# Kernel tuning notes

Hardware: AMD Instinct MI355X
Metric: run time of the kernel (lower is better)

## Reference

```python
import jax, jax.numpy as jnp
import numpy as np

BETA = 0.95
THR = 1.0
SLOPE = 25.0


@jax.custom_vjp
def spike(x):
    # heaviside(x) with fast_sigmoid surrogate gradient (slope=25)
    return (x > 0).astype(x.dtype)

def _spike_fwd(x):
    return (x > 0).astype(x.dtype), x

def _spike_bwd(x, g):
    return (g / (SLOPE * jnp.abs(x) + 1.0) ** 2,)

spike.defvjp(_spike_fwd, _spike_bwd)


def setup_inputs() -> dict:
    key = jax.random.key(0)
    ks = jax.random.split(key, 16)
    T, B, D_in, H, C = 25, 128, 2048, 4096, 1000
    P_ACTIVE = 0.1

    def sparse_layer(kw, kb, km, fan_in, fan_out):
        bound = (6.0 / fan_in) ** 0.5  # kaiming_uniform with a=sqrt(5) -> U(-sqrt(6/fan_in)*?, ...); approx scale
        w = jax.random.uniform(kw, (fan_out, fan_in), minval=-bound, maxval=bound, dtype=jnp.float32)
        mask = (jax.random.uniform(km, (fan_out, fan_in)) < P_ACTIVE).astype(jnp.float32)
        # rescale rows by sqrt(fan_in / fan_in_active) on active weights
        fan_act = jnp.clip(mask.sum(axis=1, keepdims=True), 1.0, None)
        scale = jnp.where((fan_act > 0) & (fan_act < fan_in), (fan_in / fan_act) ** 0.5, 1.0)
        w = jnp.where(mask > 0, w * scale, w)
        fan_eff = jnp.maximum(mask.sum(axis=1).mean(), 1.0)
        b_bound = 1.0 / fan_eff ** 0.5
        b = jax.random.uniform(kb, (fan_out,), minval=-b_bound, maxval=b_bound, dtype=jnp.float32)
        return w, b, mask

    w1, b1, m1 = sparse_layer(ks[0], ks[1], ks[2], D_in, H)
    w2, b2, m2 = sparse_layer(ks[3], ks[4], ks[5], H, H)
    w3, b3, m3 = sparse_layer(ks[6], ks[7], ks[8], H, H)
    bo_bound = 1.0 / H ** 0.5
    w_out = jax.random.uniform(ks[9], (C, H), minval=-bo_bound, maxval=bo_bound, dtype=jnp.float32)
    b_out = jax.random.uniform(ks[10], (C,), minval=-bo_bound, maxval=bo_bound, dtype=jnp.float32)
    x_seq = jax.random.normal(ks[11], (T, B, D_in), dtype=jnp.float32)
    return {"x_seq": x_seq, "w1": w1, "b1": b1, "m1": m1, "w2": w2, "b2": b2, "m2": m2,
            "w3": w3, "b3": b3, "m3": m3, "w_out": w_out, "b_out": b_out}


def _lif(cur, mem):
    # snntorch Leaky, reset_mechanism='subtract': reset spike from PREVIOUS mem, detached
    reset = jax.lax.stop_gradient((mem > THR).astype(mem.dtype))
    mem_new = BETA * mem + cur - reset * THR
    spk = spike(mem_new - THR)
    return spk, mem_new


def reference(x_seq, w1, b1, m1, w2, b2, m2, w3, b3, m3, w_out, b_out):
    T, B, _ = x_seq.shape
    ew1 = w1 * m1  # effective weights cached once (math identical to per-step recompute)
    ew2 = w2 * m2
    ew3 = w3 * m3

    mem1 = jnp.zeros((B, ew1.shape[0]), x_seq.dtype)
    mem2 = jnp.zeros((B, ew2.shape[0]), x_seq.dtype)
    mem3 = jnp.zeros((B, ew3.shape[0]), x_seq.dtype)
    mem_o = jnp.zeros((B, w_out.shape[0]), x_seq.dtype)
    spk_sum = jnp.zeros((B, w_out.shape[0]), x_seq.dtype)

    def step(carry, x_t):
        mem1, mem2, mem3, mem_o, spk_sum = carry
        spk1, mem1 = _lif(x_t @ ew1.T + b1, mem1)
        spk2, mem2 = _lif(spk1 @ ew2.T + b2, mem2)
        spk3, mem3 = _lif(spk2 @ ew3.T + b3, mem3)
        spk_o, mem_o = _lif(spk3 @ w_out.T + b_out, mem_o)
        return (mem1, mem2, mem3, mem_o, spk_sum + spk_o), None

    (mem1, mem2, mem3, mem_o, spk_sum), _ = jax.lax.scan(
        step, (mem1, mem2, mem3, mem_o, spk_sum), x_seq)
    return spk_sum
```

## Files before the change

kernel.cpp:

```cpp
#include <hip/hip_runtime.h>

#define T_STEPS 25
#define BATCH   128
#define D_IN    2048
#define H_DIM   4096
#define C_DIM   1000
#define N_ALL   3200
#define GEMM_Q  320
#define P_K2048 7
#define P_K4096 13
#define WOT_LD  1024

typedef __attribute__((address_space(1))) const void gas_t;
typedef __attribute__((address_space(3))) void las_t;

__device__ __forceinline__ int panel_len(int rem) {
    return (rem >= 2 * GEMM_Q) ? GEMM_Q
         : (rem > GEMM_Q ? ((rem / 2 + 15) & ~15) : rem);
}

__global__ __launch_bounds__(256)
void tmask_k(float* __restrict__ dst, const float* __restrict__ src,
             const float* __restrict__ msk, int M, int K, int MT)
{
    __shared__ float t[32][33];
    const int tx = threadIdx.x, ty = threadIdx.y;
    const int k0 = blockIdx.x * 32, m0 = blockIdx.y * 32;
    #pragma unroll
    for (int i = 0; i < 4; ++i) {
        const int m = m0 + ty + 8 * i;
        float v = 0.f;
        if (m < M) {
            const size_t gi = (size_t)m * K + k0 + tx;
            v = src[gi];
            if (msk) v *= msk[gi];
        }
        t[ty + 8 * i][tx] = v;
    }
    __syncthreads();
    const int mc = m0 + tx;
    if (mc < MT) {
        #pragma unroll
        for (int i = 0; i < 4; ++i)
            dst[(size_t)(k0 + ty + 8 * i) * MT + mc] = t[tx][ty + 8 * i];
    }
}

#define FMAQ(AS, R)                                                   \
    acc[R].x = fmaf(AS, bv.x, acc[R].x);                              \
    acc[R].y = fmaf(AS, bv.y, acc[R].y);                              \
    acc[R].z = fmaf(AS, bv.z, acc[R].z);                              \
    acc[R].w = fmaf(AS, bv.w, acc[R].w);

__global__ __launch_bounds__(256)
void gemm_w(const float* __restrict__ AT, const float* __restrict__ B,
            float* __restrict__ part, int MT, int K, int ldb, int n0)
{
#pragma clang fp reassociate(off)
    __shared__ __align__(16) float Bs[2][16][128];
    __shared__ __align__(16) float As[4][2][16][16];
    const int tid  = threadIdx.x;
    const int w    = tid >> 6;
    const int lane = tid & 63;
    const int mg   = lane >> 5;
    const int lc   = lane & 31;
    const int m0   = blockIdx.y * 64 + w * 16;
    const int p    = blockIdx.x;

    int pstart = 0, rem = K, pl = panel_len(K);
    for (int i = 0; i < p; ++i) { pstart += pl; rem -= pl; pl = panel_len(rem); }
    const int nt = pl >> 4;

    float4 acc[8];
    #pragma unroll
    for (int r = 0; r < 8; ++r) acc[r] = make_float4(0.f, 0.f, 0.f, 0.f);

    const int akr = lane >> 2, amq = (lane & 3) * 4;
    const float* ap = AT + (size_t)(pstart + akr) * MT + m0 + amq;
    const float* bsrc = B + (size_t)(pstart + w * 4 + (lane >> 5)) * ldb + n0 + lc * 4;

    {
        __builtin_amdgcn_global_load_lds((gas_t*)ap, (las_t*)&As[w][0][0][0], 16, 0, 0);
        __builtin_amdgcn_global_load_lds((gas_t*)bsrc,
                                         (las_t*)&Bs[0][w * 4][0], 16, 0, 0);
        __builtin_amdgcn_global_load_lds((gas_t*)(bsrc + 2 * (size_t)ldb),
                                         (las_t*)&Bs[0][w * 4 + 2][0], 16, 0, 0);
    }
    __syncthreads();

    for (int ti = 0; ti < nt; ++ti) {
        const int bf = ti & 1;
        if (ti + 1 < nt) {
            const float* a2 = ap + (size_t)(ti + 1) * 16 * MT;
            const float* b2 = bsrc + (size_t)(ti + 1) * 16 * ldb;
            __builtin_amdgcn_global_load_lds((gas_t*)a2, (las_t*)&As[w][bf ^ 1][0][0], 16, 0, 0);
            __builtin_amdgcn_global_load_lds((gas_t*)b2,
                                             (las_t*)&Bs[bf ^ 1][w * 4][0], 16, 0, 0);
            __builtin_amdgcn_global_load_lds((gas_t*)(b2 + 2 * (size_t)ldb),
                                             (las_t*)&Bs[bf ^ 1][w * 4 + 2][0], 16, 0, 0);
        }
        {
            float4 a0 = *(const float4*)&As[w][bf][0][mg * 8];
            float4 a1 = *(const float4*)&As[w][bf][0][mg * 8 + 4];
            float4 bv = *(const float4*)&Bs[bf][0][lc * 4];
            #pragma unroll
            for (int kk = 0; kk < 16; ++kk) {
                float4 na0, na1, nbv;
                if (kk < 15) {
                    na0 = *(const float4*)&As[w][bf][kk + 1][mg * 8];
                    na1 = *(const float4*)&As[w][bf][kk + 1][mg * 8 + 4];
                    nbv = *(const float4*)&Bs[bf][kk + 1][lc * 4];
                }
                FMAQ(a0.x, 0) FMAQ(a0.y, 1) FMAQ(a0.z, 2) FMAQ(a0.w, 3)
                FMAQ(a1.x, 4) FMAQ(a1.y, 5) FMAQ(a1.z, 6) FMAQ(a1.w, 7)
                if (kk < 15) { a0 = na0; a1 = na1; bv = nbv; }
            }
        }
        __syncthreads();
    }

    const int mrow0 = m0 + mg * 8;
    #pragma unroll
    for (int r = 0; r < 8; ++r)
        *(float4*)&part[((size_t)p * MT + mrow0 + r) * BATCH + lc * 4] = acc[r];
}

__device__ __forceinline__ float lif1e(float c, float& m)
{
    const float r = (m > 1.0f) ? 1.0f : 0.0f;
    const float mn = __fsub_rn(__fadd_rn(__fmul_rn(0.95f, m), c), r);
    m = mn;
    return (mn > 1.0f) ? 1.0f : 0.0f;
}

__global__ __launch_bounds__(256)
void reduce_lif4(const float* __restrict__ part, int P, int Mdim,
                 const float* __restrict__ bias, float* __restrict__ mem,
                 float* __restrict__ spk)
{
#pragma clang fp reassociate(off)
    const int idx4 = blockIdx.x * 256 + threadIdx.x;
    const int idx = idx4 * 4;
    const size_t stride = (size_t)Mdim * BATCH;
    float4 tot = *(const float4*)&part[idx];
    for (int z = 1; z < P; ++z) {
        const float4 pv = *(const float4*)&part[(size_t)z * stride + idx];
        tot.x = __fadd_rn(tot.x, pv.x); tot.y = __fadd_rn(tot.y, pv.y);
        tot.z = __fadd_rn(tot.z, pv.z); tot.w = __fadd_rn(tot.w, pv.w);
    }
    const float bb = bias[idx >> 7];
    float4 mm = *(float4*)&mem[idx];
    float4 sp;
    sp.x = lif1e(__fadd_rn(tot.x, bb), mm.x);
    sp.y = lif1e(__fadd_rn(tot.y, bb), mm.y);
    sp.z = lif1e(__fadd_rn(tot.z, bb), mm.z);
    sp.w = lif1e(__fadd_rn(tot.w, bb), mm.w);
    *(float4*)&mem[idx] = mm;
    *(float4*)&spk[idx] = sp;
}

__global__ __launch_bounds__(256)
void reduce_lif_out4(const float* __restrict__ part, int P, int Mpad,
                     const float* __restrict__ bias, float* __restrict__ mem,
                     float* __restrict__ out)
{
#pragma clang fp reassociate(off)
    const int idx4 = blockIdx.x * 256 + threadIdx.x;
    if (idx4 >= (C_DIM * BATCH) / 4) return;
    const int idx = idx4 * 4;
    const int cc = idx >> 7, b = idx & 127;
    const size_t stride = (size_t)Mpad * BATCH;
    float4 tot = *(const float4*)&part[idx];
    for (int z = 1; z < P; ++z) {
        const float4 pv = *(const float4*)&part[(size_t)z * stride + idx];
        tot.x = __fadd_rn(tot.x, pv.x); tot.y = __fadd_rn(tot.y, pv.y);
        tot.z = __fadd_rn(tot.z, pv.z); tot.w = __fadd_rn(tot.w, pv.w);
    }
    const float bb = bias[cc];
    float4 mm = *(float4*)&mem[idx];
    float s;
    s = lif1e(__fadd_rn(tot.x, bb), mm.x); if (s > 0.f) out[(size_t)(b+0) * C_DIM + cc] += 1.0f;
    s = lif1e(__fadd_rn(tot.y, bb), mm.y); if (s > 0.f) out[(size_t)(b+1) * C_DIM + cc] += 1.0f;
    s = lif1e(__fadd_rn(tot.z, bb), mm.z); if (s > 0.f) out[(size_t)(b+2) * C_DIM + cc] += 1.0f;
    s = lif1e(__fadd_rn(tot.w, bb), mm.w); if (s > 0.f) out[(size_t)(b+3) * C_DIM + cc] += 1.0f;
    *(float4*)&mem[idx] = mm;
}

extern "C" void kernel_launch(void* const* d_in, const int* in_sizes, int n_in,
                              void* d_out, int out_size, void* d_ws, size_t ws_size,
                              hipStream_t stream)
{
    const float* x  = (const float*)d_in[0];
    const float* w1 = (const float*)d_in[1];
    const float* b1 = (const float*)d_in[2];
    const float* m1 = (const float*)d_in[3];
    const float* w2 = (const float*)d_in[4];
    const float* b2 = (const float*)d_in[5];
    const float* m2 = (const float*)d_in[6];
    const float* w3 = (const float*)d_in[7];
    const float* b3 = (const float*)d_in[8];
    const float* m3 = (const float*)d_in[9];
    const float* wo = (const float*)d_in[10];
    const float* bo = (const float*)d_in[11];
    float* out = (float*)d_out;
    float* ws  = (float*)d_ws;
    (void)in_sizes; (void)n_in; (void)ws_size;

    const size_t HB = (size_t)H_DIM * BATCH;
    const size_t CB = (size_t)C_DIM * BATCH;

    size_t off = 0;
    const size_t MEM1 = off; off += HB;
    const size_t MEM2 = off; off += HB;
    const size_t MEM3 = off; off += HB;
    const size_t MEMO = off; off += CB;
    const size_t stateFloats = off;
    const size_t SPK1 = off; off += HB;
    const size_t SPK2 = off; off += HB;
    const size_t SPK3 = off; off += HB;
    const size_t PART = off; off += (size_t)P_K4096 * HB;
    const size_t EWT1 = off; off += (size_t)D_IN * H_DIM;
    const size_t EWT2 = off; off += (size_t)H_DIM * H_DIM;
    const size_t EWT3 = off; off += (size_t)H_DIM * H_DIM;
    const size_t WOT  = off; off += (size_t)H_DIM * WOT_LD;
    const size_t XT   = off; off += (size_t)D_IN * N_ALL;

    hipMemsetAsync(d_ws, 0, stateFloats * sizeof(float), stream);
    hipMemsetAsync(d_out, 0, (size_t)out_size * sizeof(float), stream);

    {
        dim3 tb(32, 8);
        tmask_k<<<dim3(D_IN / 32, H_DIM / 32), tb, 0, stream>>>(ws + EWT1, w1, m1, H_DIM, D_IN, H_DIM);
        tmask_k<<<dim3(H_DIM / 32, H_DIM / 32), tb, 0, stream>>>(ws + EWT2, w2, m2, H_DIM, H_DIM, H_DIM);
        tmask_k<<<dim3(H_DIM / 32, H_DIM / 32), tb, 0, stream>>>(ws + EWT3, w3, m3, H_DIM, H_DIM, H_DIM);
        tmask_k<<<dim3(H_DIM / 32, WOT_LD / 32), tb, 0, stream>>>(ws + WOT, wo, nullptr, C_DIM, H_DIM, WOT_LD);
        tmask_k<<<dim3(D_IN / 32, N_ALL / 32), tb, 0, stream>>>(ws + XT, x, nullptr, N_ALL, D_IN, N_ALL);
    }

    const dim3 g1(P_K2048, H_DIM / 64);
    const dim3 g23(P_K4096, H_DIM / 64);
    const dim3 go(P_K4096, WOT_LD / 64);
    const int gLif4  = (int)(HB / 4 / 256);
    const int gLifO4 = (int)((CB / 4 + 255) / 256);

    for (int t = 0; t < T_STEPS; ++t) {
        gemm_w<<<g1, 256, 0, stream>>>(ws + EWT1, ws + XT, ws + PART,
                                       H_DIM, D_IN, N_ALL, t * BATCH);
        reduce_lif4<<<gLif4, 256, 0, stream>>>(ws + PART, P_K2048, H_DIM, b1, ws + MEM1, ws + SPK1);

        gemm_w<<<g23, 256, 0, stream>>>(ws + EWT2, ws + SPK1, ws + PART,
                                        H_DIM, H_DIM, BATCH, 0);
        reduce_lif4<<<gLif4, 256, 0, stream>>>(ws + PART, P_K4096, H_DIM, b2, ws + MEM2, ws + SPK2);

        gemm_w<<<g23, 256, 0, stream>>>(ws + EWT3, ws + SPK2, ws + PART,
                                        H_DIM, H_DIM, BATCH, 0);
        reduce_lif4<<<gLif4, 256, 0, stream>>>(ws + PART, P_K4096, H_DIM, b3, ws + MEM3, ws + SPK3);

        gemm_w<<<go, 256, 0, stream>>>(ws + WOT, ws + SPK3, ws + PART,
                                       WOT_LD, H_DIM, BATCH, 0);
        reduce_lif_out4<<<gLifO4, 256, 0, stream>>>(ws + PART, P_K4096, WOT_LD, bo, ws + MEMO, out);
    }
}
```

Baseline: 5.164 ms.

## Co-launch next step's layer-1 GEMM with output GEMM and pair their reductions

Layer 1 depends only on the input sequence, so its GEMM for step t+1 is merged into one launch with the output-layer GEMM of step t. Their reduce/LIF kernels are likewise merged into one launch. The aim is to fill the GPU better, since the output GEMM has few blocks, and to cut per-step launch count. This needs a separate partial buffer region for the output layer so the two partial sums do not collide. It also adds a prologue GEMM before the loop and an epilogue reduction after it.

```diff
diff --git a/kernel.cpp b/kernel.cpp
--- a/kernel.cpp
+++ b/kernel.cpp
@@ -52,20 +52,23 @@
     acc[R].z = fmaf(AS, bv.z, acc[R].z);                              \
     acc[R].w = fmaf(AS, bv.w, acc[R].w);
 
-__global__ __launch_bounds__(256)
-void gemm_w(const float* __restrict__ AT, const float* __restrict__ B,
-            float* __restrict__ part, int MT, int K, int ldb, int n0)
+typedef float BsT[16][128];
+typedef float AsT[2][16][16];
+
+__device__ __forceinline__ void gemm_body(BsT* Bs, AsT* As,
+                                          const float* __restrict__ AT,
+                                          const float* __restrict__ B,
+                                          float* __restrict__ part,
+                                          int MT, int K, int ldb, int n0,
+                                          int p, int my)
 {
 #pragma clang fp reassociate(off)
-    __shared__ __align__(16) float Bs[2][16][128];
-    __shared__ __align__(16) float As[4][2][16][16];
     const int tid  = threadIdx.x;
     const int w    = tid >> 6;
     const int lane = tid & 63;
     const int mg   = lane >> 5;
     const int lc   = lane & 31;
-    const int m0   = blockIdx.y * 64 + w * 16;
-    const int p    = blockIdx.x;
+    const int m0   = my * 64 + w * 16;
 
     int pstart = 0, rem = K, pl = panel_len(K);
     for (int i = 0; i < p; ++i) { pstart += pl; rem -= pl; pl = panel_len(rem); }
@@ -125,6 +128,33 @@
         *(float4*)&part[((size_t)p * MT + mrow0 + r) * BATCH + lc * 4] = acc[r];
 }
 
+__global__ __launch_bounds__(256)
+void gemm_w(const float* __restrict__ AT, const float* __restrict__ B,
+            float* __restrict__ part, int MT, int K, int ldb, int n0)
+{
+    __shared__ __align__(16) float BsS[2][16][128];
+    __shared__ __align__(16) float AsS[4][2][16][16];
+    gemm_body((BsT*)BsS, (AsT*)AsS, AT, B, part, MT, K, ldb, n0,
+              blockIdx.x, blockIdx.y);
+}
+
+__global__ __launch_bounds__(256)
+void gemm_pair(const float* __restrict__ ATo, const float* __restrict__ Bo,
+               float* __restrict__ po, int MTo, int Ko, int ldbo, int n0o, int nbo, int npo,
+               const float* __restrict__ AT1, const float* __restrict__ B1,
+               float* __restrict__ p1, int MT1, int K1, int ldb1, int n01, int np1)
+{
+    __shared__ __align__(16) float BsS[2][16][128];
+    __shared__ __align__(16) float AsS[4][2][16][16];
+    const int bid = blockIdx.x;
+    if (bid < nbo)
+        gemm_body((BsT*)BsS, (AsT*)AsS, ATo, Bo, po, MTo, Ko, ldbo, n0o,
+                  bid % npo, bid / npo);
+    else
+        gemm_body((BsT*)BsS, (AsT*)AsS, AT1, B1, p1, MT1, K1, ldb1, n01,
+                  (bid - nbo) % np1, (bid - nbo) / np1);
+}
+
 __device__ __forceinline__ float lif1e(float c, float& m)
 {
     const float r = (m > 1.0f) ? 1.0f : 0.0f;
@@ -133,13 +163,12 @@
     return (mn > 1.0f) ? 1.0f : 0.0f;
 }
 
-__global__ __launch_bounds__(256)
-void reduce_lif4(const float* __restrict__ part, int P, int Mdim,
-                 const float* __restrict__ bias, float* __restrict__ mem,
-                 float* __restrict__ spk)
+__device__ __forceinline__ void red_lif4_body(int bid, const float* __restrict__ part,
+                                              int P, int Mdim, const float* __restrict__ bias,
+                                              float* __restrict__ mem, float* __restrict__ spk)
 {
 #pragma clang fp reassociate(off)
-    const int idx4 = blockIdx.x * 256 + threadIdx.x;
+    const int idx4 = bid * 256 + threadIdx.x;
     const int idx = idx4 * 4;
     const size_t stride = (size_t)Mdim * BATCH;
     float4 tot = *(const float4*)&part[idx];
@@ -159,13 +188,12 @@
     *(float4*)&spk[idx] = sp;
 }
 
-__global__ __launch_bounds__(256)
-void reduce_lif_out4(const float* __restrict__ part, int P, int Mpad,
-                     const float* __restrict__ bias, float* __restrict__ mem,
-                     float* __restrict__ out)
+__device__ __forceinline__ void red_lifo_body(int bid, const float* __restrict__ part,
+                                              int P, int Mpad, const float* __restrict__ bias,
+                                              float* __restrict__ mem, float* __restrict__ out)
 {
 #pragma clang fp reassociate(off)
-    const int idx4 = blockIdx.x * 256 + threadIdx.x;
+    const int idx4 = bid * 256 + threadIdx.x;
     if (idx4 >= (C_DIM * BATCH) / 4) return;
     const int idx = idx4 * 4;
     const int cc = idx >> 7, b = idx & 127;
@@ -184,6 +212,32 @@
     s = lif1e(__fadd_rn(tot.z, bb), mm.z); if (s > 0.f) out[(size_t)(b+2) * C_DIM + cc] += 1.0f;
     s = lif1e(__fadd_rn(tot.w, bb), mm.w); if (s > 0.f) out[(size_t)(b+3) * C_DIM + cc] += 1.0f;
     *(float4*)&mem[idx] = mm;
+}
+
+__global__ __launch_bounds__(256)
+void reduce_lif4(const float* __restrict__ part, int P, int Mdim,
+                 const float* __restrict__ bias, float* __restrict__ mem,
+                 float* __restrict__ spk)
+{ red_lif4_body(blockIdx.x, part, P, Mdim, bias, mem, spk); }
+
+__global__ __launch_bounds__(256)
+void reduce_lif_out4(const float* __restrict__ part, int P, int Mpad,
+                     const float* __restrict__ bias, float* __restrict__ mem,
+                     float* __restrict__ out)
+{ red_lifo_body(blockIdx.x, part, P, Mpad, bias, mem, out); }
+
+__global__ __launch_bounds__(256)
+void reduce_pair(const float* __restrict__ part, int P, int Mdim,
+                 const float* __restrict__ bias, float* __restrict__ mem,
+                 float* __restrict__ spk,
+                 const float* __restrict__ parto, int Po, int Mpad,
+                 const float* __restrict__ biaso, float* __restrict__ memo,
+                 float* __restrict__ outp, int nb1)
+{
+    if ((int)blockIdx.x < nb1)
+        red_lif4_body(blockIdx.x, part, P, Mdim, bias, mem, spk);
+    else
+        red_lifo_body(blockIdx.x - nb1, parto, Po, Mpad, biaso, memo, outp);
 }
 
 extern "C" void kernel_launch(void* const* d_in, const int* in_sizes, int n_in,
@@ -219,6 +273,7 @@
     const size_t SPK2 = off; off += HB;
     const size_t SPK3 = off; off += HB;
     const size_t PART = off; off += (size_t)P_K4096 * HB;
+    const size_t PARTO = PART + (size_t)P_K2048 * HB;
     const size_t EWT1 = off; off += (size_t)D_IN * H_DIM;
     const size_t EWT2 = off; off += (size_t)H_DIM * H_DIM;
     const size_t EWT3 = off; off += (size_t)H_DIM * H_DIM;
@@ -242,22 +297,31 @@
     const dim3 go(P_K4096, WOT_LD / 64);
     const int gLif4  = (int)(HB / 4 / 256);
     const int gLifO4 = (int)((CB / 4 + 255) / 256);
+    const int NB_OUT = P_K4096 * (WOT_LD / 64);
+    const int NB_L1  = P_K2048 * (H_DIM / 64);
+
+    gemm_w<<<g1, 256, 0, stream>>>(ws + EWT1, ws + XT, ws + PART, H_DIM, D_IN, N_ALL, 0);
 
     for (int t = 0; t < T_STEPS; ++t) {
-        gemm_w<<<g1, 256, 0, stream>>>(ws + EWT1, ws + XT, ws + PART,
-                                       H_DIM, D_IN, N_ALL, t * BATCH);
-        reduce_lif4<<<gLif4, 256, 0, stream>>>(ws + PART, P_K2048, H_DIM, b1, ws + MEM1, ws + SPK1);
-
-        gemm_w<<<g23, 256, 0, stream>>>(ws + EWT2, ws + SPK1, ws + PART,
-                                        H_DIM, H_DIM, BATCH, 0);
+        if (t == 0)
+            reduce_lif4<<<gLif4, 256, 0, stream>>>(ws + PART, P_K2048, H_DIM, b1, ws + MEM1, ws + SPK1);
+        else
+            reduce_pair<<<gLif4 + gLifO4, 256, 0, stream>>>(
+                ws + PART, P_K2048, H_DIM, b1, ws + MEM1, ws + SPK1,
+                ws + PARTO, P_K4096, WOT_LD, bo, ws + MEMO, out, gLif4);
+
+        gemm_w<<<g23, 256, 0, stream>>>(ws + EWT2, ws + SPK1, ws + PART, H_DIM, H_DIM, BATCH, 0);
         reduce_lif4<<<gLif4, 256, 0, stream>>>(ws + PART, P_K4096, H_DIM, b2, ws + MEM2, ws + SPK2);
 
-        gemm_w<<<g23, 256, 0, stream>>>(ws + EWT3, ws + SPK2, ws + PART,
-                                        H_DIM, H_DIM, BATCH, 0);
+        gemm_w<<<g23, 256, 0, stream>>>(ws + EWT3, ws + SPK2, ws + PART, H_DIM, H_DIM, BATCH, 0);
         reduce_lif4<<<gLif4, 256, 0, stream>>>(ws + PART, P_K4096, H_DIM, b3, ws + MEM3, ws + SPK3);
 
-        gemm_w<<<go, 256, 0, stream>>>(ws + WOT, ws + SPK3, ws + PART,
-                                       WOT_LD, H_DIM, BATCH, 0);
-        reduce_lif_out4<<<gLifO4, 256, 0, stream>>>(ws + PART, P_K4096, WOT_LD, bo, ws + MEMO, out);
-    }
-}
+        if (t + 1 < T_STEPS)
+            gemm_pair<<<NB_OUT + NB_L1, 256, 0, stream>>>(
+                ws + WOT, ws + SPK3, ws + PARTO, WOT_LD, H_DIM, BATCH, 0, NB_OUT, P_K4096,
+                ws + EWT1, ws + XT, ws + PART, H_DIM, D_IN, N_ALL, (t + 1) * BATCH, P_K2048);
+        else
+            gemm_w<<<go, 256, 0, stream>>>(ws + WOT, ws + SPK3, ws + PARTO, WOT_LD, H_DIM, BATCH, 0);
+    }
+    reduce_lif_out4<<<gLifO4, 256, 0, stream>>>(ws + PARTO, P_K4096, WOT_LD, bo, ws + MEMO, out);
+}
```

Measured after the change: 4.666 ms. 9.6% less time.
